# Kernel optimization log

Measured on AMD Instinct MI355X. Metric: run time of the kernel, lower is better.

Reference implementation:

```python
import jax, jax.numpy as jnp
import numpy as np

N_WORDS = 30000
EMB_DIM = 784  # 28*28
MAT_DIM = 28
BATCH = 1024
SEQ_LEN = 64


def setup_inputs() -> dict:
    key = jax.random.key(0)
    k_sent, k_tab = jax.random.split(key)
    # token ids in [0, n_words]; row 0 is the neutral (identity) / padding element
    sent = jax.random.randint(k_sent, (BATCH, SEQ_LEN), 0, N_WORDS + 1, dtype=jnp.int32).astype(jnp.int64)
    eye_flat = jnp.eye(MAT_DIM, dtype=jnp.float32).reshape(-1)
    # 'identity' init strategy: identity + small gaussian noise (scale kept small for stability of long products)
    table = eye_flat + 0.01 * jax.random.normal(k_tab, (N_WORDS + 1, EMB_DIM), dtype=jnp.float32)
    table = table.at[0].set(eye_flat)  # neutral element at padding_idx=0
    return {"sent": sent, "table": table}


def reference(sent, table):
    # sent: [B, S] int ids; table: [n_words+1, d*d]
    B, S = sent.shape
    d = MAT_DIM
    word_mats = table[sent].reshape(B, S, d, d)  # embedding lookup + unflatten
    # CMOW: continual multiplication cur = cur @ W_i, sequential over seq dim
    init = word_mats[:, 0]                      # [B, d, d]
    rest = jnp.moveaxis(word_mats[:, 1:], 1, 0)  # [S-1, B, d, d]

    def step(cur, w):
        return jnp.matmul(cur, w), None

    cur, _ = jax.lax.scan(step, init, rest)
    return cur.reshape(B, d * d)  # flatten matrix back to embedding
```

## Files before the change

### kernel.cpp

```cpp
#include <hip/hip_runtime.h>
#include <stdint.h>

#define SEQ 64
#define D 28
#define EMB 784
#define CH 8
#define BUFF 832

typedef float float4v __attribute__((ext_vector_type(4)));

__device__ __forceinline__ void dma_row(const float* grow, float* lbuf, int lane)
{
    const char* g16 = (const char*)grow + lane * 16;
    const char* g4  = (const char*)grow + 3072 + lane * 4;
    char* l = (char*)lbuf;
    __builtin_amdgcn_global_load_lds((const __attribute__((address_space(1))) void*)(g16),
                                     (__attribute__((address_space(3))) void*)(l), 16, 0, 0);
    __builtin_amdgcn_global_load_lds((const __attribute__((address_space(1))) void*)(g16 + 1024),
                                     (__attribute__((address_space(3))) void*)(l + 1024), 16, 0, 0);
    __builtin_amdgcn_global_load_lds((const __attribute__((address_space(1))) void*)(g16 + 2048),
                                     (__attribute__((address_space(3))) void*)(l + 2048), 16, 0, 0);
    __builtin_amdgcn_global_load_lds((const __attribute__((address_space(1))) void*)(g4),
                                     (__attribute__((address_space(3))) void*)(l + 3072), 4, 0, 0);
}

__device__ __forceinline__ void xpose_write(const float4v ct[4],
                                            float* __restrict__ LTw,
                                            int it, int jt)
{
#pragma unroll
    for (int c = 0; c < 4; ++c) {
        float4v t;
        t.x = ct[0][c]; t.y = ct[1][c]; t.z = ct[2][c]; t.w = ct[3][c];
        *(float4v*)&LTw[(4 * jt + c) * D + 4 * it] = t;
    }
}

template <int CNT, typename F>
__device__ __forceinline__ void mat_chain(F rowptr, float* __restrict__ LTw,
                                          float* __restrict__ B0,
                                          float* __restrict__ B1,
                                          float4v ct[4], int it, int jt, int lane)
{
    dma_row(rowptr(1), B1, lane);

#pragma unroll 1
    for (int j = 1; j < CNT; ++j) {
        const int jn = (j + 1 < CNT) ? (j + 1) : j;
        float* nB = (j & 1) ? B0 : B1;
        float* cB = (j & 1) ? B1 : B0;
        dma_row(rowptr(jn), nB, lane);

        xpose_write(ct, LTw, it, jt);

        __builtin_amdgcn_sched_barrier(0);
        __builtin_amdgcn_s_waitcnt(0x0074);
        __builtin_amdgcn_sched_barrier(0);

        const float* ap = LTw + 4 * it;
        const float* bp = cB + 4 * jt;
        float4v acc[4] = {};
#pragma unroll
        for (int k = 0; k < 28; ++k) {
            float4v av = *(const float4v*)(ap + k * D);
            float4v bb = *(const float4v*)(bp + k * D);
#pragma unroll
            for (int r = 0; r < 4; ++r) acc[r] += bb * av[r];
        }
#pragma unroll
        for (int r = 0; r < 4; ++r) ct[r] = acc[r];
    }
}

__global__ __launch_bounds__(256, 1) void w2m_leaf(
    const int* __restrict__ sent,
    const float* __restrict__ table,
    float* __restrict__ ws0)
{
    __shared__ float LT[4 * EMB] __attribute__((aligned(16)));
    __shared__ float BB[4 * 2 * BUFF] __attribute__((aligned(16)));
    const int lane = threadIdx.x & 63;
    const int wid  = threadIdx.x >> 6;
    const int w = blockIdx.x * 4 + wid;
    const int b = w >> 3;
    const int g = w & 7;
    int it = lane / 7, jt = lane % 7;
    const bool act = lane < 49;
    if (!act) { it = 6; jt = 6; }
    float* LTw = &LT[wid * EMB];
    float* Bw0 = &BB[wid * 2 * BUFF];
    float* Bw1 = Bw0 + BUFF;

    const int myidx = sent[b * SEQ + 8 * g + (lane & 7)];
    int jl[CH];
#pragma unroll
    for (int j = 0; j < CH; ++j) jl[j] = __builtin_amdgcn_readlane(myidx, j);

    const float* row0 = table + (size_t)jl[0] * EMB;
    float4v ct[4];
#pragma unroll
    for (int r = 0; r < 4; ++r)
        ct[r] = *(const float4v*)(row0 + (4 * it + r) * D + 4 * jt);

    mat_chain<CH>([&](int j) { return table + (size_t)jl[j] * EMB; },
                  LTw, Bw0, Bw1, ct, it, jt, lane);

    if (act) {
        float* orow = ws0 + (size_t)w * EMB;
#pragma unroll
        for (int r = 0; r < 4; ++r)
            *(float4v*)(orow + (4 * it + r) * D + 4 * jt) = ct[r];
    }
}

__global__ __launch_bounds__(64, 1) void w2m_top(
    const float* __restrict__ ws0,
    float* __restrict__ out)
{
    __shared__ float LT[EMB] __attribute__((aligned(16)));
    __shared__ float BB[2 * BUFF] __attribute__((aligned(16)));
    const int lane = threadIdx.x;
    const int b = blockIdx.x;
    int it = lane / 7, jt = lane % 7;
    const bool act = lane < 49;
    if (!act) { it = 6; jt = 6; }

    const float* base = ws0 + (size_t)b * CH * EMB;
    float4v ct[4];
#pragma unroll
    for (int r = 0; r < 4; ++r)
        ct[r] = *(const float4v*)(base + (4 * it + r) * D + 4 * jt);

    mat_chain<CH>([&](int j) { return base + (size_t)j * EMB; },
                  LT, &BB[0], &BB[BUFF], ct, it, jt, lane);

    if (act) {
        float* orow = out + (size_t)b * EMB;
#pragma unroll
        for (int r = 0; r < 4; ++r)
            *(float4v*)(orow + (4 * it + r) * D + 4 * jt) = ct[r];
    }
}

__global__ __launch_bounds__(64, 1) void w2m_serial(
    const int* __restrict__ sent,
    const float* __restrict__ table,
    float* __restrict__ out)
{
    __shared__ float LT[EMB] __attribute__((aligned(16)));
    __shared__ float BB[2 * BUFF] __attribute__((aligned(16)));
    const int lane = threadIdx.x;
    const int b = blockIdx.x;
    int it = lane / 7, jt = lane % 7;
    const bool act = lane < 49;
    if (!act) { it = 6; jt = 6; }

    const int myidx = sent[b * SEQ + lane];
    int jl[SEQ];
#pragma unroll
    for (int s = 0; s < SEQ; ++s) jl[s] = __builtin_amdgcn_readlane(myidx, s);

    const float* row0 = table + (size_t)jl[0] * EMB;
    float4v ct[4];
#pragma unroll
    for (int r = 0; r < 4; ++r)
        ct[r] = *(const float4v*)(row0 + (4 * it + r) * D + 4 * jt);

    mat_chain<SEQ>([&](int s) { return table + (size_t)jl[s] * EMB; },
                   LT, &BB[0], &BB[BUFF], ct, it, jt, lane);

    if (act) {
        float* orow = out + (size_t)b * EMB;
#pragma unroll
        for (int r = 0; r < 4; ++r)
            *(float4v*)(orow + (4 * it + r) * D + 4 * jt) = ct[r];
    }
}

extern "C" void kernel_launch(void* const* d_in, const int* in_sizes, int n_in,
                              void* d_out, int out_size, void* d_ws, size_t ws_size,
                              hipStream_t stream) {
    const int* sent = (const int*)d_in[0];
    const float* table = (const float*)d_in[1];
    float* out = (float*)d_out;
    const int batch = in_sizes[0] / SEQ;
    const size_t ws_needed = (size_t)batch * CH * EMB * sizeof(float);

    if (ws_size >= ws_needed) {
        float* ws0 = (float*)d_ws;
        const int waves1 = batch * CH;
        hipLaunchKernelGGL(w2m_leaf, dim3(waves1 / 4), dim3(256), 0, stream,
                           sent, table, ws0);
        hipLaunchKernelGGL(w2m_top, dim3(batch), dim3(64), 0, stream,
                           ws0, out);
    } else {
        hipLaunchKernelGGL(w2m_serial, dim3(batch), dim3(64), 0, stream,
                           sent, table, out);
    }
}
```

Baseline: 180.0 us.

## Use split-bf16 MFMA for leaf-level matrix chain products

Replaces the scalar FMA leaf kernel with one that runs each 28x28 product as four 16x16x32 bf16 MFMA tiles. Each fp32 operand is split into high and low bf16 parts, and three MFMAs per tile approximate fp32 accuracy. Zero padding covers the k range from 28 to 32. The intent is to move the dominant leaf matmul work onto matrix cores. It adds split and transpose overhead and slightly lower precision, and it reads DMA buffer padding beyond row 28.

```diff
diff --git a/kernel.cpp b/kernel.cpp
--- a/kernel.cpp
+++ b/kernel.cpp
@@ -6,8 +6,31 @@
 #define EMB 784
 #define CH 8
 #define BUFF 832
+#define BUFW 1024
+#define CTW 36
+#define CTSZ (32 * CTW)
 
 typedef float float4v __attribute__((ext_vector_type(4)));
+typedef __bf16 bf16x8 __attribute__((ext_vector_type(8)));
+
+union FragU { unsigned u[4]; bf16x8 v; };
+
+__device__ __forceinline__ unsigned fbits(float x) { union { float f; unsigned u; } t; t.f = x; return t.u; }
+__device__ __forceinline__ float fof(unsigned u) { union { unsigned u; float f; } t; t.u = u; return t.f; }
+
+__device__ __forceinline__ void split_frags(const float x[8], bf16x8& hi, bf16x8& lo)
+{
+    FragU H, L;
+#pragma unroll
+    for (int p = 0; p < 4; ++p) {
+        unsigned ua = fbits(x[2 * p]), ub = fbits(x[2 * p + 1]);
+        H.u[p] = (ua >> 16) | (ub & 0xFFFF0000u);
+        unsigned la = fbits(x[2 * p]     - fof(ua & 0xFFFF0000u));
+        unsigned lb = fbits(x[2 * p + 1] - fof(ub & 0xFFFF0000u));
+        L.u[p] = (la >> 16) | (lb & 0xFFFF0000u);
+    }
+    hi = H.v; lo = L.v;
+}
 
 __device__ __forceinline__ void dma_row(const float* grow, float* lbuf, int lane)
 {
@@ -24,15 +47,119 @@
                                      (__attribute__((address_space(3))) void*)(l + 3072), 4, 0, 0);
 }
 
+__global__ __launch_bounds__(256, 1) void w2m_leaf_mfma(
+    const int* __restrict__ sent,
+    const float* __restrict__ table,
+    float* __restrict__ ws0)
+{
+    __shared__ float CT[4 * CTSZ] __attribute__((aligned(16)));
+    __shared__ float BB[4 * 2 * BUFW] __attribute__((aligned(16)));
+    const int lane = threadIdx.x & 63;
+    const int wid  = threadIdx.x >> 6;
+    const int w = blockIdx.x * 4 + wid;
+    const int b = w >> 3;
+    const int g = w & 7;
+    const int c = lane & 15;
+    const int quad = lane >> 4;
+    const bool q3 = (quad == 3);
+    float* CTw = &CT[wid * CTSZ];
+    float* B0 = &BB[wid * 2 * BUFW];
+    float* B1 = B0 + BUFW;
+
+    const int myidx = sent[b * SEQ + 8 * g + (lane & 7)];
+    int jl[CH];
+#pragma unroll
+    for (int j = 0; j < CH; ++j) jl[j] = __builtin_amdgcn_readlane(myidx, j);
+
+    dma_row(table + (size_t)jl[0] * EMB, B0, lane);
+    dma_row(table + (size_t)jl[1] * EMB, B1, lane);
+    __builtin_amdgcn_s_waitcnt(0x0074);
+
+    float4v acc[2][2];
+#pragma unroll
+    for (int R = 0; R < 2; ++R)
+#pragma unroll
+        for (int Cc = 0; Cc < 2; ++Cc)
+#pragma unroll
+            for (int i = 0; i < 4; ++i)
+                acc[R][Cc][i] = B0[(16 * R + 4 * quad + i) * D + 16 * Cc + c];
+    __builtin_amdgcn_s_waitcnt(0xC07F);
+
+#pragma unroll 1
+    for (int j = 1; j < CH; ++j) {
+        const int jn = (j + 1 < CH) ? (j + 1) : j;
+        float* nB = (j & 1) ? B0 : B1;
+        float* cB = (j & 1) ? B1 : B0;
+        dma_row(table + (size_t)jl[jn] * EMB, nB, lane);
+
+#pragma unroll
+        for (int R = 0; R < 2; ++R)
+#pragma unroll
+            for (int Cc = 0; Cc < 2; ++Cc)
+#pragma unroll
+                for (int i = 0; i < 4; ++i)
+                    CTw[(16 * R + 4 * quad + i) * CTW + 16 * Cc + c] = acc[R][Cc][i];
+
+        __builtin_amdgcn_sched_barrier(0);
+        __builtin_amdgcn_s_waitcnt(0x0074);
+        __builtin_amdgcn_sched_barrier(0);
+
+        bf16x8 Ah[2], Al[2];
+#pragma unroll
+        for (int R = 0; R < 2; ++R) {
+            const float* ap = CTw + (16 * R + c) * CTW + 8 * quad;
+            float4v x0 = *(const float4v*)ap;
+            float4v x1 = *(const float4v*)(ap + 4);
+            if (q3) x1 = float4v{0.f, 0.f, 0.f, 0.f};
+            float x[8] = {x0.x, x0.y, x0.z, x0.w, x1.x, x1.y, x1.z, x1.w};
+            split_frags(x, Ah[R], Al[R]);
+        }
+
+        bf16x8 Bh[2], Bl[2];
+#pragma unroll
+        for (int Cc = 0; Cc < 2; ++Cc) {
+            const float* bp = cB + (8 * quad) * D + 16 * Cc + c;
+            float x[8];
+#pragma unroll
+            for (int t = 0; t < 8; ++t) x[t] = bp[t * D];
+            if (q3) { x[4] = 0.f; x[5] = 0.f; x[6] = 0.f; x[7] = 0.f; }
+            split_frags(x, Bh[Cc], Bl[Cc]);
+        }
+
+#pragma unroll
+        for (int R = 0; R < 2; ++R)
+#pragma unroll
+            for (int Cc = 0; Cc < 2; ++Cc) {
+                float4v d = {0.f, 0.f, 0.f, 0.f};
+                d = __builtin_amdgcn_mfma_f32_16x16x32_bf16(Ah[R], Bh[Cc], d, 0, 0, 0);
+                d = __builtin_amdgcn_mfma_f32_16x16x32_bf16(Ah[R], Bl[Cc], d, 0, 0, 0);
+                d = __builtin_amdgcn_mfma_f32_16x16x32_bf16(Al[R], Bh[Cc], d, 0, 0, 0);
+                acc[R][Cc] = d;
+            }
+    }
+
+    float* orow = ws0 + (size_t)w * EMB;
+#pragma unroll
+    for (int R = 0; R < 2; ++R)
+#pragma unroll
+        for (int Cc = 0; Cc < 2; ++Cc)
+#pragma unroll
+            for (int i = 0; i < 4; ++i) {
+                const int row = 16 * R + 4 * quad + i;
+                const int col = 16 * Cc + c;
+                if (row < D && col < D) orow[row * D + col] = acc[R][Cc][i];
+            }
+}
+
 __device__ __forceinline__ void xpose_write(const float4v ct[4],
                                             float* __restrict__ LTw,
                                             int it, int jt)
 {
 #pragma unroll
-    for (int c = 0; c < 4; ++c) {
+    for (int cc = 0; cc < 4; ++cc) {
         float4v t;
-        t.x = ct[0][c]; t.y = ct[1][c]; t.z = ct[2][c]; t.w = ct[3][c];
-        *(float4v*)&LTw[(4 * jt + c) * D + 4 * it] = t;
+        t.x = ct[0][cc]; t.y = ct[1][cc]; t.z = ct[2][cc]; t.w = ct[3][cc];
+        *(float4v*)&LTw[(4 * jt + cc) * D + 4 * it] = t;
     }
 }
 
@@ -72,53 +199,12 @@
     }
 }
 
-__global__ __launch_bounds__(256, 1) void w2m_leaf(
-    const int* __restrict__ sent,
-    const float* __restrict__ table,
-    float* __restrict__ ws0)
-{
-    __shared__ float LT[4 * EMB] __attribute__((aligned(16)));
-    __shared__ float BB[4 * 2 * BUFF] __attribute__((aligned(16)));
-    const int lane = threadIdx.x & 63;
-    const int wid  = threadIdx.x >> 6;
-    const int w = blockIdx.x * 4 + wid;
-    const int b = w >> 3;
-    const int g = w & 7;
-    int it = lane / 7, jt = lane % 7;
-    const bool act = lane < 49;
-    if (!act) { it = 6; jt = 6; }
-    float* LTw = &LT[wid * EMB];
-    float* Bw0 = &BB[wid * 2 * BUFF];
-    float* Bw1 = Bw0 + BUFF;
-
-    const int myidx = sent[b * SEQ + 8 * g + (lane & 7)];
-    int jl[CH];
-#pragma unroll
-    for (int j = 0; j < CH; ++j) jl[j] = __builtin_amdgcn_readlane(myidx, j);
-
-    const float* row0 = table + (size_t)jl[0] * EMB;
-    float4v ct[4];
-#pragma unroll
-    for (int r = 0; r < 4; ++r)
-        ct[r] = *(const float4v*)(row0 + (4 * it + r) * D + 4 * jt);
-
-    mat_chain<CH>([&](int j) { return table + (size_t)jl[j] * EMB; },
-                  LTw, Bw0, Bw1, ct, it, jt, lane);
-
-    if (act) {
-        float* orow = ws0 + (size_t)w * EMB;
-#pragma unroll
-        for (int r = 0; r < 4; ++r)
-            *(float4v*)(orow + (4 * it + r) * D + 4 * jt) = ct[r];
-    }
-}
-
 __global__ __launch_bounds__(64, 1) void w2m_top(
     const float* __restrict__ ws0,
     float* __restrict__ out)
 {
     __shared__ float LT[EMB] __attribute__((aligned(16)));
-    __shared__ float BB[2 * BUFF] __attribute__((aligned(16)));
+    __shared__ float BBt[2 * BUFF] __attribute__((aligned(16)));
     const int lane = threadIdx.x;
     const int b = blockIdx.x;
     int it = lane / 7, jt = lane % 7;
@@ -132,7 +218,7 @@
         ct[r] = *(const float4v*)(base + (4 * it + r) * D + 4 * jt);
 
     mat_chain<CH>([&](int j) { return base + (size_t)j * EMB; },
-                  LT, &BB[0], &BB[BUFF], ct, it, jt, lane);
+                  LT, &BBt[0], &BBt[BUFF], ct, it, jt, lane);
 
     if (act) {
         float* orow = out + (size_t)b * EMB;
@@ -148,7 +234,7 @@
     float* __restrict__ out)
 {
     __shared__ float LT[EMB] __attribute__((aligned(16)));
-    __shared__ float BB[2 * BUFF] __attribute__((aligned(16)));
+    __shared__ float BBs[2 * BUFF] __attribute__((aligned(16)));
     const int lane = threadIdx.x;
     const int b = blockIdx.x;
     int it = lane / 7, jt = lane % 7;
@@ -156,18 +242,18 @@
     if (!act) { it = 6; jt = 6; }
 
     const int myidx = sent[b * SEQ + lane];
-    int jl[SEQ];
-#pragma unroll
-    for (int s = 0; s < SEQ; ++s) jl[s] = __builtin_amdgcn_readlane(myidx, s);
-
-    const float* row0 = table + (size_t)jl[0] * EMB;
+    int jls[SEQ];
+#pragma unroll
+    for (int s = 0; s < SEQ; ++s) jls[s] = __builtin_amdgcn_readlane(myidx, s);
+
+    const float* row0 = table + (size_t)jls[0] * EMB;
     float4v ct[4];
 #pragma unroll
     for (int r = 0; r < 4; ++r)
         ct[r] = *(const float4v*)(row0 + (4 * it + r) * D + 4 * jt);
 
-    mat_chain<SEQ>([&](int s) { return table + (size_t)jl[s] * EMB; },
-                   LT, &BB[0], &BB[BUFF], ct, it, jt, lane);
+    mat_chain<SEQ>([&](int s) { return table + (size_t)jls[s] * EMB; },
+                   LT, &BBs[0], &BBs[BUFF], ct, it, jt, lane);
 
     if (act) {
         float* orow = out + (size_t)b * EMB;
@@ -189,7 +275,7 @@
     if (ws_size >= ws_needed) {
         float* ws0 = (float*)d_ws;
         const int waves1 = batch * CH;
-        hipLaunchKernelGGL(w2m_leaf, dim3(waves1 / 4), dim3(256), 0, stream,
+        hipLaunchKernelGGL(w2m_leaf_mfma, dim3(waves1 / 4), dim3(256), 0, stream,
                            sent, table, ws0);
         hipLaunchKernelGGL(w2m_top, dim3(batch), dim3(64), 0, stream,
                            ws0, out);
```

Result: faster. 169.7 us (-5.7%).
